# Optimization experiments

Measured on AMD Instinct MI355X. Metric: run time of the kernel, lower is better.

The kernel has to match this reference:

```python
import jax, jax.numpy as jnp
import numpy as np

B, N, E, H = 8, 512, 256, 8
DK = E // H
DIST_BAR = (0.3, 0.7, 1e10)  # init dist_bar + [1e10] appended in forward
NEG = -1e10


def setup_inputs() -> dict:
    key = jax.random.key(0)
    ks = jax.random.split(key, 24)
    s = 0.02
    inp = {
        'query': jax.random.normal(ks[0], (B, N, E), jnp.float32),
        'key':   jax.random.normal(ks[1], (B, N, E), jnp.float32),
        'value': jax.random.normal(ks[2], (B, N, E), jnp.float32),
        'dist':  jax.random.uniform(ks[3], (B, N, N), jnp.float32),
        'mask':  jax.random.randint(ks[4], (B, N, N), 0, 2).astype(jnp.int32),
        # 4 linears (q, k, v, out), stored as [in, out] for x @ W
        'Wq': jax.random.normal(ks[5], (E, E)) * s, 'bq': jnp.zeros((E,)),
        'Wk': jax.random.normal(ks[6], (E, E)) * s, 'bk': jnp.zeros((E,)),
        'Wv': jax.random.normal(ks[7], (E, E)) * s, 'bv': jnp.zeros((E,)),
        'Wo': jax.random.normal(ks[8], (E, E)) * s, 'bo': jnp.zeros((E,)),
        # cnn: Conv2d(1,H,1) -> ReLU -> Conv2d(H,H,1); 1x1 convs = per-pixel linear maps
        'cw1': jax.random.normal(ks[9], (H,)) * s,     'cb1': jnp.zeros((H,)),
        'cw2': jax.random.normal(ks[10], (H, H)) * s,  'cb2': jnp.zeros((H,)),
        # scale_linear: Linear(3E, E) -> ReLU -> Linear(E, E)
        'Ws1': jax.random.normal(ks[11], (3 * E, E)) * s, 'bs1': jnp.zeros((E,)),
        'Ws2': jax.random.normal(ks[12], (E, E)) * s,     'bs2': jnp.zeros((E,)),
    }
    return inp


def reference(query, key, value, dist, mask,
              Wq, bq, Wk, bk, Wv, bv, Wo, bo,
              cw1, cb1, cw2, cb2, Ws1, bs1, Ws2, bs2):
    def heads(x, W, b):  # [B,N,E] -> [B,H,N,DK]
        return (x @ W + b).reshape(B, N, H, DK).transpose(0, 2, 1, 3)

    q, k, v = heads(query, Wq, bq), heads(key, Wk, bk), heads(value, Wv, bv)
    d4 = dist[:, None]  # [B,1,N,N]
    # 1x1 conv stack: [B,1,N,N] -> [B,H,N,N]
    c1 = jax.nn.relu(d4 * cw1[None, :, None, None] + cb1[None, :, None, None])
    dist_conv = jnp.einsum('oi,bijk->bojk', cw2, c1) + cb2[None, :, None, None]

    scores = jnp.einsum('bhqd,bhkd->bhqk', q, k) / np.sqrt(DK).astype(np.float32)
    scores = scores * dist_conv
    scores = jnp.where(mask[:, None] == 0, NEG, scores)

    outs = []
    for bar in DIST_BAR:
        dm = d4 < bar                       # [B,1,N,N] bool
        dm = dm.at[:, :, 0, :].set(True).at[:, :, :, 0].set(True)
        s = jnp.where(dm, scores, NEG)
        p = jax.nn.softmax(s, axis=-1)      # [B,H,N,N]
        o = jnp.einsum('bhqk,bhkd->bhqd', p, v)
        o = o.transpose(0, 2, 1, 3).reshape(B, N, E)
        outs.append(o @ Wo + bo)
    x = jnp.concatenate(outs, axis=-1)      # [B,N,3E]
    h1 = jax.nn.relu(x @ Ws1 + bs1)
    return h1 @ Ws2 + bs2                   # [B,N,E]
```

## Files before the change

kernel.cpp:

```cpp
#include <hip/hip_runtime.h>
#include <math.h>

typedef _Float16 h16;
typedef __attribute__((ext_vector_type(8))) _Float16 h16x8;
typedef __attribute__((ext_vector_type(4))) float f32x4;
typedef unsigned long long u64t;
typedef unsigned int u32t;
typedef unsigned short u16t;
typedef unsigned char u8t;

__global__ void bcomb_k(const float* __restrict__ bo, const float* __restrict__ Ws1,
                        const float* __restrict__ bs1, float* __restrict__ bcomb)
{
    const int jj = threadIdx.x;
    const int r0 = blockIdx.x * 64;
    float acc = (blockIdx.x == 0) ? bs1[jj] : 0.f;
    for (int r = r0; r < r0 + 64; ++r)
        acc = fmaf(bo[r & 255], Ws1[(size_t)r * 256 + jj], acc);
    atomicAdd(&bcomb[jj], acc);
}

__global__ __launch_bounds__(256) void transpose_k(
    const float* __restrict__ Wq, const float* __restrict__ Wk,
    const float* __restrict__ Wv, const float* __restrict__ Ws2,
    const float* __restrict__ Ws1, h16* __restrict__ WT)
{
    const int z = blockIdx.z;
    const float* in = (z == 0) ? Wq : (z == 1) ? Wk : (z == 2) ? Wv :
                      (z == 3) ? Ws2 : (Ws1 + (size_t)(z - 4) * 65536);
    h16* out = WT + (size_t)z * 65536;
    __shared__ float T[32][33];
    const int t = threadIdx.x, tx = t & 31, ty = t >> 5;
    const int r0 = blockIdx.x * 32, c0 = blockIdx.y * 32;
    #pragma unroll
    for (int i = 0; i < 4; ++i) {
        const int row = ty + i * 8;
        T[row][tx] = in[(size_t)(r0 + row) * 256 + c0 + tx];
    }
    __syncthreads();
    #pragma unroll
    for (int i = 0; i < 4; ++i) {
        const int row = ty + i * 8;
        out[(size_t)(c0 + row) * 256 + r0 + tx] = (h16)T[tx][row];
    }
}

template<int A_F32, int MODE>
__global__ __launch_bounds__(256) void hgemm_k(
    const void* __restrict__ Av, const h16* __restrict__ Bt0,
    const float* __restrict__ bias, void* __restrict__ outv,
    int M, int Nn, int K, long btz, int ldt)
{
    const h16* Bt = Bt0 + (size_t)blockIdx.z * btz;
    __shared__ __align__(16) h16 As[64][40];
    __shared__ __align__(16) h16 Bs[64][40];
    const int t = threadIdx.x, w = t >> 6, lane = t & 63;
    const int Q = lane >> 4, n = lane & 15;
    const int row0 = blockIdx.x * 64, col0 = blockIdx.y * 64;
    const int sr = t >> 2, sc = (t & 3) * 8;
    f32x4 acc[4];
    #pragma unroll
    for (int c = 0; c < 4; ++c) acc[c] = (f32x4){0.f, 0.f, 0.f, 0.f};

    for (int k0 = 0; k0 < K; k0 += 32) {
        __syncthreads();
        if (A_F32) {
            const float* ap = (const float*)Av + (size_t)(row0 + sr) * K + k0 + sc;
            float4 f0 = *(const float4*)ap;
            float4 f1 = *(const float4*)(ap + 4);
            h16x8 hv;
            hv[0] = (h16)f0.x; hv[1] = (h16)f0.y; hv[2] = (h16)f0.z; hv[3] = (h16)f0.w;
            hv[4] = (h16)f1.x; hv[5] = (h16)f1.y; hv[6] = (h16)f1.z; hv[7] = (h16)f1.w;
            *(h16x8*)&As[sr][sc] = hv;
        } else {
            *(h16x8*)&As[sr][sc] =
                *(const h16x8*)((const h16*)Av + (size_t)(row0 + sr) * K + k0 + sc);
        }
        *(h16x8*)&Bs[sr][sc] = *(const h16x8*)(Bt + (size_t)(col0 + sr) * K + k0 + sc);
        __syncthreads();
        h16x8 af = *(const h16x8*)&As[w * 16 + n][Q * 8];
        #pragma unroll
        for (int c = 0; c < 4; ++c) {
            h16x8 bf = *(const h16x8*)&Bs[c * 16 + n][Q * 8];
            acc[c] = __builtin_amdgcn_mfma_f32_16x16x32_f16(af, bf, acc[c], 0, 0, 0);
        }
    }

    float bvv[4] = {0.f, 0.f, 0.f, 0.f};
    if (MODE != 4) {
        #pragma unroll
        for (int c = 0; c < 4; ++c) bvv[c] = bias[col0 + c * 16 + n];
    }
    #pragma unroll
    for (int c = 0; c < 4; ++c) {
        #pragma unroll
        for (int r = 0; r < 4; ++r) {
            const int row = row0 + w * 16 + 4 * Q + r;
            const int col = col0 + c * 16 + n;
            if (MODE == 0) {
                ((float*)outv)[(size_t)row * Nn + col] = acc[c][r] + bvv[c];
            } else if (MODE == 2) {
                ((h16*)outv)[(size_t)row * Nn + col] = (h16)fmaxf(acc[c][r] + bvv[c], 0.f);
            } else {
                ((h16*)outv)[(size_t)col * ldt + (int)blockIdx.z * M + row] = (h16)acc[c][r];
            }
        }
    }
}

__global__ __launch_bounds__(256) void qkv_hgemm_k(
    const float* __restrict__ Xq, const float* __restrict__ Xk,
    const float* __restrict__ Xv, const h16* __restrict__ WT,
    const float* __restrict__ bq, const float* __restrict__ bk,
    const float* __restrict__ bv,
    h16* __restrict__ qb, h16* __restrict__ kb, h16* __restrict__ vbT)
{
    const int z = blockIdx.z;
    const float* A    = (z == 0) ? Xq : (z == 1) ? Xk : Xv;
    const h16*   Bt   = WT + (size_t)z * 65536;
    const float* bias = (z == 0) ? bq : (z == 1) ? bk : bv;

    __shared__ __align__(16) h16 As[64][40];
    __shared__ __align__(16) h16 Bs[64][40];
    const int t = threadIdx.x, w = t >> 6, lane = t & 63;
    const int Q = lane >> 4, n = lane & 15;
    const int row0 = blockIdx.x * 64, col0 = blockIdx.y * 64;
    const int sr = t >> 2, sc = (t & 3) * 8;
    f32x4 acc[4];
    #pragma unroll
    for (int c = 0; c < 4; ++c) acc[c] = (f32x4){0.f, 0.f, 0.f, 0.f};

    for (int k0 = 0; k0 < 256; k0 += 32) {
        __syncthreads();
        {
            const float* ap = A + (size_t)(row0 + sr) * 256 + k0 + sc;
            float4 f0 = *(const float4*)ap;
            float4 f1 = *(const float4*)(ap + 4);
            h16x8 hv;
            hv[0] = (h16)f0.x; hv[1] = (h16)f0.y; hv[2] = (h16)f0.z; hv[3] = (h16)f0.w;
            hv[4] = (h16)f1.x; hv[5] = (h16)f1.y; hv[6] = (h16)f1.z; hv[7] = (h16)f1.w;
            *(h16x8*)&As[sr][sc] = hv;
            *(h16x8*)&Bs[sr][sc] = *(const h16x8*)(Bt + (size_t)(col0 + sr) * 256 + k0 + sc);
        }
        __syncthreads();
        h16x8 af = *(const h16x8*)&As[w * 16 + n][Q * 8];
        #pragma unroll
        for (int c = 0; c < 4; ++c) {
            h16x8 bf = *(const h16x8*)&Bs[c * 16 + n][Q * 8];
            acc[c] = __builtin_amdgcn_mfma_f32_16x16x32_f16(af, bf, acc[c], 0, 0, 0);
        }
    }

    float bvv[4];
    #pragma unroll
    for (int c = 0; c < 4; ++c) bvv[c] = bias[col0 + c * 16 + n];

    if (z < 2) {
        h16* out = z ? kb : qb;
        #pragma unroll
        for (int c = 0; c < 4; ++c)
            #pragma unroll
            for (int r = 0; r < 4; ++r)
                out[(size_t)(row0 + w * 16 + 4 * Q + r) * 256 + col0 + c * 16 + n] =
                    (h16)(acc[c][r] + bvv[c]);
    } else {
        const int bb = row0 >> 9;
        #pragma unroll
        for (int c = 0; c < 4; ++c)
            #pragma unroll
            for (int r = 0; r < 4; ++r) {
                const int m = row0 + w * 16 + 4 * Q + r;
                const int col = col0 + c * 16 + n;
                vbT[((size_t)(bb * 256 + col)) * 512 + (m & 511)] = (h16)(acc[c][r] + bvv[c]);
            }
    }
}

__global__ __launch_bounds__(256, 4) void attn_k(
    const h16* __restrict__ qb, const h16* __restrict__ kb,
    const h16* __restrict__ vbT,
    const float* __restrict__ dist, const int* __restrict__ mask,
    const float* __restrict__ cw1, const float* __restrict__ cb1,
    const float* __restrict__ cw2, const float* __restrict__ cb2,
    h16* __restrict__ OB)
{
    const int bx = blockIdx.x, b = bx >> 5, q0 = (bx & 31) * 16;
    const int t = threadIdx.x, w = t >> 6, lane = t & 63;
    const int Q = lane >> 4, n = lane & 15;
    const int h = blockIdx.y * 4 + w;

    __shared__ __align__(16) h16 c1t[16][65][8];
    __shared__ __align__(16) u8t Cd[16][72];
    __shared__ __align__(16) h16 Sx[4][16][72];

    const float invs = 0.17677669529663687f;
    float w1[8], b1[8], w2w[8];
    #pragma unroll
    for (int u = 0; u < 8; ++u) {
        w1[u] = cw1[u]; b1[u] = cb1[u];
        w2w[u] = invs * cw2[h * 8 + u];
    }
    const float fb = invs * cb2[h];

    const h16x8 aq =
        *(const h16x8*)(qb + ((size_t)(b * 512 + q0 + n)) * 256 + h * 32 + Q * 8);

    const f32x4 z4 = {0.f, 0.f, 0.f, 0.f};
    f32x4 acc[3][2];
    #pragma unroll
    for (int s = 0; s < 3; ++s) { acc[s][0] = z4; acc[s][1] = z4; }
    float mprev = -3e38f;
    float lsum[3] = {0.f, 0.f, 0.f};

    const int scol = t & 63, srow0 = t >> 6;

    for (int kc = 0; kc < 8; ++kc) {
        const int kk0 = kc * 64;
        __syncthreads();
        #pragma unroll
        for (int i = 0; i < 4; ++i) {
            const int row = srow0 + 4 * i;
            const size_t off = ((size_t)(b * 512 + q0 + row)) * 512 + kk0 + scol;
            const float d = dist[off];
            const int mk = mask[off];
            const bool fr = ((q0 + row) == 0) || ((kk0 + scol) == 0);
            const bool keep = (mk != 0);
            const u32t code = (keep && (fr || d < 0.3f) ? 1u : 0u)
                            | (keep && (fr || d < 0.7f) ? 2u : 0u)
                            | (keep ? 4u : 0u);
            Cd[row][scol] = (u8t)code;
            h16x8 ch;
            #pragma unroll
            for (int u = 0; u < 8; ++u)
                ch[u] = (h16)fmaxf(fmaf(d, w1[u], b1[u]), 0.f);
            *(h16x8*)&c1t[row][scol][0] = ch;
        }
        __syncthreads();

        f32x4 s4[4];
        #pragma unroll
        for (int cg = 0; cg < 4; ++cg) {
            h16x8 kf = *(const h16x8*)(
                kb + ((size_t)(b * 512 + kk0 + cg * 16 + n)) * 256 + h * 32 + Q * 8);
            s4[cg] = __builtin_amdgcn_mfma_f32_16x16x32_f16(aq, kf, z4, 0, 0, 0);
        }
        #pragma unroll
        for (int cg = 0; cg < 4; ++cg) {
            #pragma unroll
            for (int r = 0; r < 4; ++r) {
                h16x8 ch = *(const h16x8*)&c1t[4 * Q + r][cg * 16 + n][0];
                float f = fb;
                #pragma unroll
                for (int u = 0; u < 8; ++u)
                    f = fmaf((float)ch[u], w2w[u], f);
                Sx[w][4 * Q + r][cg * 16 + n] = (h16)(s4[cg][r] * f);
            }
        }
        __builtin_amdgcn_wave_barrier();

        float sv[16];
        u64t cd0 = *(const u64t*)&Cd[n][Q * 8];
        u64t cd1 = *(const u64t*)&Cd[n][32 + Q * 8];
        {
            h16x8 sh0 = *(const h16x8*)&Sx[w][n][Q * 8];
            h16x8 sh1 = *(const h16x8*)&Sx[w][n][32 + Q * 8];
            #pragma unroll
            for (int j = 0; j < 8; ++j) { sv[j] = (float)sh0[j]; sv[8 + j] = (float)sh1[j]; }
        }
        float cm = -3e38f;
        #pragma unroll
        for (int i = 0; i < 16; ++i) {
            const u32t cc = (u32t)((i < 8 ? cd0 : cd1) >> (8 * (i & 7))) & 7u;
            cm = fmaxf(cm, (cc & 4u) ? sv[i] : -3e38f);
        }
        cm = fmaxf(cm, __shfl_xor(cm, 16));
        cm = fmaxf(cm, __shfl_xor(cm, 32));
        const float mnew = fmaxf(mprev, cm);
        const float alphaA = __expf(mprev - mnew);
        mprev = mnew;

        #pragma unroll
        for (int r = 0; r < 4; ++r) {
            const float aR = __shfl(alphaA, 4 * Q + r);
            #pragma unroll
            for (int s = 0; s < 3; ++s) { acc[s][0][r] *= aR; acc[s][1][r] *= aR; }
        }

        h16x8 pf[3][2];
        float l0 = 0.f, l1 = 0.f, l2 = 0.f;
        #pragma unroll
        for (int i = 0; i < 16; ++i) {
            const u32t cc = (u32t)((i < 8 ? cd0 : cd1) >> (8 * (i & 7))) & 7u;
            const float e = __expf(sv[i] - mnew);
            const float p0 = (cc & 1u) ? e : 0.f;
            const float p1 = (cc & 2u) ? e : 0.f;
            const float p2 = (cc & 4u) ? e : 0.f;
            l0 += p0; l1 += p1; l2 += p2;
            pf[0][i >> 3][i & 7] = (h16)p0;
            pf[1][i >> 3][i & 7] = (h16)p1;
            pf[2][i >> 3][i & 7] = (h16)p2;
        }
        lsum[0] = lsum[0] * alphaA + l0;
        lsum[1] = lsum[1] * alphaA + l1;
        lsum[2] = lsum[2] * alphaA + l2;

        #pragma unroll
        for (int kb2 = 0; kb2 < 2; ++kb2) {
            #pragma unroll
            for (int nh = 0; nh < 2; ++nh) {
                h16x8 vf = *(const h16x8*)(
                    vbT + ((size_t)((b * 8 + h) * 32 + nh * 16 + n)) * 512
                        + kk0 + kb2 * 32 + Q * 8);
                #pragma unroll
                for (int s = 0; s < 3; ++s)
                    acc[s][nh] = __builtin_amdgcn_mfma_f32_16x16x32_f16(
                        pf[s][kb2], vf, acc[s][nh], 0, 0, 0);
            }
        }
    }

    float lrow[3];
    #pragma unroll
    for (int s = 0; s < 3; ++s) {
        float lv = lsum[s];
        lv += __shfl_xor(lv, 16);
        lv += __shfl_xor(lv, 32);
        lrow[s] = lv;
    }
    #pragma unroll
    for (int s = 0; s < 3; ++s) {
        #pragma unroll
        for (int r = 0; r < 4; ++r) {
            const float il = 1.0f / __shfl(lrow[s], 4 * Q + r);
            const size_t row = (size_t)(b * 512 + q0 + 4 * Q + r);
            h16* op = OB + row * 768 + s * 256 + h * 32 + n;
            op[0]  = (h16)(acc[s][0][r] * il);
            op[16] = (h16)(acc[s][1][r] * il);
        }
    }
}

extern "C" void kernel_launch(void* const* d_in, const int* in_sizes, int n_in,
                              void* d_out, int out_size, void* d_ws, size_t ws_size,
                              hipStream_t stream)
{
    const float* query = (const float*)d_in[0];
    const float* key   = (const float*)d_in[1];
    const float* value = (const float*)d_in[2];
    const float* dist  = (const float*)d_in[3];
    const int*   mask  = (const int*)d_in[4];
    const float* Wq = (const float*)d_in[5];  const float* bq = (const float*)d_in[6];
    const float* Wk = (const float*)d_in[7];  const float* bk = (const float*)d_in[8];
    const float* Wv = (const float*)d_in[9];  const float* bv = (const float*)d_in[10];
    const float* Wo = (const float*)d_in[11]; const float* bo = (const float*)d_in[12];
    const float* cw1 = (const float*)d_in[13]; const float* cb1 = (const float*)d_in[14];
    const float* cw2 = (const float*)d_in[15]; const float* cb2 = (const float*)d_in[16];
    const float* Ws1 = (const float*)d_in[17]; const float* bs1 = (const float*)d_in[18];
    const float* Ws2 = (const float*)d_in[19]; const float* bs2 = (const float*)d_in[20];

    h16* qb    = (h16*)d_ws;
    h16* kb    = qb + 1048576;
    h16* vbT   = kb + 1048576;
    h16* OB    = vbT + 1048576;
    h16* h1    = OB + 3145728;
    h16* WT    = h1 + 1048576;
    h16* WbigT = WT + 458752;
    float* bcomb = (float*)(WbigT + 196608);

    hipMemsetAsync(bcomb, 0, 256 * sizeof(float), stream);
    bcomb_k<<<dim3(12), dim3(256), 0, stream>>>(bo, Ws1, bs1, bcomb);

    transpose_k<<<dim3(8, 8, 7), 256, 0, stream>>>(Wq, Wk, Wv, Ws2, Ws1, WT);

    hgemm_k<1, 4><<<dim3(4, 4, 3), 256, 0, stream>>>(
        Wo, WT + 4 * 65536, nullptr, WbigT, 256, 256, 256, 65536, 768);

    qkv_hgemm_k<<<dim3(64, 4, 3), 256, 0, stream>>>(
        query, key, value, WT, bq, bk, bv, qb, kb, vbT);

    attn_k<<<dim3(256, 2), 256, 0, stream>>>(
        qb, kb, vbT, dist, mask, cw1, cb1, cw2, cb2, OB);

    hgemm_k<0, 2><<<dim3(64, 4, 1), 256, 0, stream>>>(
        OB, WbigT, bcomb, h1, 4096, 256, 768, 0, 0);
    hgemm_k<0, 0><<<dim3(64, 4, 1), 256, 0, stream>>>(
        h1, WT + 3 * 65536, bs2, d_out, 4096, 256, 256, 0, 0);
}
```

Before: 193.2 us.

## Merge weight prep and QKV projection into one launch, register-pipeline attention

Drops the separate transpose, bias-combine, memset and weight-fold kernels. Their work now runs inside one merged single-wave-per-block launch that reads the fp32 weights directly with strided per-element loads. The attention kernel no longer stages dist/mask codes and conv features in shared memory with block barriers. It computes the conv factor per element in registers and prefetches the next chunk's K, V, dist and mask into registers, with a double-buffered per-wave score scratch. The final two GEMMs become LDS-free 64-thread kernels. This cuts launch count and block-level synchronisation, but uncoalesced strided weight loads, more conv arithmetic per element, and lower occupancy (launch bounds 256,2) could offset the gains.

```diff
diff --git a/kernel.cpp b/kernel.cpp
--- a/kernel.cpp
+++ b/kernel.cpp
@@ -3,180 +3,116 @@
 
 typedef _Float16 h16;
 typedef __attribute__((ext_vector_type(8))) _Float16 h16x8;
+typedef __attribute__((ext_vector_type(4))) _Float16 h16x4;
 typedef __attribute__((ext_vector_type(4))) float f32x4;
-typedef unsigned long long u64t;
 typedef unsigned int u32t;
-typedef unsigned short u16t;
-typedef unsigned char u8t;
-
-__global__ void bcomb_k(const float* __restrict__ bo, const float* __restrict__ Ws1,
-                        const float* __restrict__ bs1, float* __restrict__ bcomb)
-{
-    const int jj = threadIdx.x;
-    const int r0 = blockIdx.x * 64;
-    float acc = (blockIdx.x == 0) ? bs1[jj] : 0.f;
-    for (int r = r0; r < r0 + 64; ++r)
-        acc = fmaf(bo[r & 255], Ws1[(size_t)r * 256 + jj], acc);
-    atomicAdd(&bcomb[jj], acc);
-}
-
-__global__ __launch_bounds__(256) void transpose_k(
-    const float* __restrict__ Wq, const float* __restrict__ Wk,
-    const float* __restrict__ Wv, const float* __restrict__ Ws2,
-    const float* __restrict__ Ws1, h16* __restrict__ WT)
-{
-    const int z = blockIdx.z;
-    const float* in = (z == 0) ? Wq : (z == 1) ? Wk : (z == 2) ? Wv :
-                      (z == 3) ? Ws2 : (Ws1 + (size_t)(z - 4) * 65536);
-    h16* out = WT + (size_t)z * 65536;
-    __shared__ float T[32][33];
-    const int t = threadIdx.x, tx = t & 31, ty = t >> 5;
-    const int r0 = blockIdx.x * 32, c0 = blockIdx.y * 32;
-    #pragma unroll
-    for (int i = 0; i < 4; ++i) {
-        const int row = ty + i * 8;
-        T[row][tx] = in[(size_t)(r0 + row) * 256 + c0 + tx];
-    }
-    __syncthreads();
-    #pragma unroll
-    for (int i = 0; i < 4; ++i) {
-        const int row = ty + i * 8;
-        out[(size_t)(c0 + row) * 256 + r0 + tx] = (h16)T[tx][row];
-    }
-}
-
-template<int A_F32, int MODE>
-__global__ __launch_bounds__(256) void hgemm_k(
-    const void* __restrict__ Av, const h16* __restrict__ Bt0,
-    const float* __restrict__ bias, void* __restrict__ outv,
-    int M, int Nn, int K, long btz, int ldt)
-{
-    const h16* Bt = Bt0 + (size_t)blockIdx.z * btz;
-    __shared__ __align__(16) h16 As[64][40];
-    __shared__ __align__(16) h16 Bs[64][40];
-    const int t = threadIdx.x, w = t >> 6, lane = t & 63;
+
+__global__ __launch_bounds__(64) void k1_k(
+    const float* __restrict__ query, const float* __restrict__ key,
+    const float* __restrict__ value,
+    const float* __restrict__ Wq, const float* __restrict__ bq,
+    const float* __restrict__ Wk, const float* __restrict__ bk,
+    const float* __restrict__ Wv, const float* __restrict__ bv,
+    const float* __restrict__ Wo, const float* __restrict__ bo,
+    const float* __restrict__ Ws1, const float* __restrict__ bs1,
+    h16* __restrict__ qb, h16* __restrict__ kb, h16* __restrict__ vbT,
+    h16* __restrict__ WbigT, float* __restrict__ bcomb)
+{
+    const int bid = blockIdx.x, lane = threadIdx.x;
     const int Q = lane >> 4, n = lane & 15;
-    const int row0 = blockIdx.x * 64, col0 = blockIdx.y * 64;
-    const int sr = t >> 2, sc = (t & 3) * 8;
-    f32x4 acc[4];
-    #pragma unroll
-    for (int c = 0; c < 4; ++c) acc[c] = (f32x4){0.f, 0.f, 0.f, 0.f};
-
-    for (int k0 = 0; k0 < K; k0 += 32) {
-        __syncthreads();
-        if (A_F32) {
-            const float* ap = (const float*)Av + (size_t)(row0 + sr) * K + k0 + sc;
-            float4 f0 = *(const float4*)ap;
-            float4 f1 = *(const float4*)(ap + 4);
-            h16x8 hv;
-            hv[0] = (h16)f0.x; hv[1] = (h16)f0.y; hv[2] = (h16)f0.z; hv[3] = (h16)f0.w;
-            hv[4] = (h16)f1.x; hv[5] = (h16)f1.y; hv[6] = (h16)f1.z; hv[7] = (h16)f1.w;
-            *(h16x8*)&As[sr][sc] = hv;
+    const f32x4 z4 = {0.f, 0.f, 0.f, 0.f};
+
+    if (bid < 3072) {
+        const int z = bid >> 10, tt = bid & 1023;
+        const int row0 = (tt & 255) << 4, col0 = (tt >> 8) << 6;
+        const float* A    = (z == 0) ? query : (z == 1) ? key : value;
+        const float* W    = (z == 0) ? Wq : (z == 1) ? Wk : Wv;
+        const float* bias = (z == 0) ? bq : (z == 1) ? bk : bv;
+
+        f32x4 acc[4] = {z4, z4, z4, z4};
+        #pragma unroll 2
+        for (int k0 = 0; k0 < 256; k0 += 32) {
+            const float* ap = A + (size_t)(row0 + n) * 256 + k0 + Q * 8;
+            float4 a0 = *(const float4*)ap, a1 = *(const float4*)(ap + 4);
+            h16x8 af;
+            af[0] = (h16)a0.x; af[1] = (h16)a0.y; af[2] = (h16)a0.z; af[3] = (h16)a0.w;
+            af[4] = (h16)a1.x; af[5] = (h16)a1.y; af[6] = (h16)a1.z; af[7] = (h16)a1.w;
+            #pragma unroll
+            for (int cg = 0; cg < 4; ++cg) {
+                const int col = col0 + cg * 16 + n;
+                h16x8 bf;
+                #pragma unroll
+                for (int j = 0; j < 8; ++j)
+                    bf[j] = (h16)W[(size_t)(k0 + Q * 8 + j) * 256 + col];
+                acc[cg] = __builtin_amdgcn_mfma_f32_16x16x32_f16(af, bf, acc[cg], 0, 0, 0);
+            }
+        }
+        if (z < 2) {
+            h16* out = z ? kb : qb;
+            #pragma unroll
+            for (int cg = 0; cg < 4; ++cg) {
+                const int col = col0 + cg * 16 + n;
+                const float bvv = bias[col];
+                #pragma unroll
+                for (int r = 0; r < 4; ++r)
+                    out[(size_t)(row0 + 4 * Q + r) * 256 + col] = (h16)(acc[cg][r] + bvv);
+            }
         } else {
-            *(h16x8*)&As[sr][sc] =
-                *(const h16x8*)((const h16*)Av + (size_t)(row0 + sr) * K + k0 + sc);
-        }
-        *(h16x8*)&Bs[sr][sc] = *(const h16x8*)(Bt + (size_t)(col0 + sr) * K + k0 + sc);
-        __syncthreads();
-        h16x8 af = *(const h16x8*)&As[w * 16 + n][Q * 8];
-        #pragma unroll
-        for (int c = 0; c < 4; ++c) {
-            h16x8 bf = *(const h16x8*)&Bs[c * 16 + n][Q * 8];
-            acc[c] = __builtin_amdgcn_mfma_f32_16x16x32_f16(af, bf, acc[c], 0, 0, 0);
-        }
-    }
-
-    float bvv[4] = {0.f, 0.f, 0.f, 0.f};
-    if (MODE != 4) {
-        #pragma unroll
-        for (int c = 0; c < 4; ++c) bvv[c] = bias[col0 + c * 16 + n];
-    }
-    #pragma unroll
-    for (int c = 0; c < 4; ++c) {
-        #pragma unroll
-        for (int r = 0; r < 4; ++r) {
-            const int row = row0 + w * 16 + 4 * Q + r;
-            const int col = col0 + c * 16 + n;
-            if (MODE == 0) {
-                ((float*)outv)[(size_t)row * Nn + col] = acc[c][r] + bvv[c];
-            } else if (MODE == 2) {
-                ((h16*)outv)[(size_t)row * Nn + col] = (h16)fmaxf(acc[c][r] + bvv[c], 0.f);
-            } else {
-                ((h16*)outv)[(size_t)col * ldt + (int)blockIdx.z * M + row] = (h16)acc[c][r];
-            }
-        }
-    }
-}
-
-__global__ __launch_bounds__(256) void qkv_hgemm_k(
-    const float* __restrict__ Xq, const float* __restrict__ Xk,
-    const float* __restrict__ Xv, const h16* __restrict__ WT,
-    const float* __restrict__ bq, const float* __restrict__ bk,
-    const float* __restrict__ bv,
-    h16* __restrict__ qb, h16* __restrict__ kb, h16* __restrict__ vbT)
-{
-    const int z = blockIdx.z;
-    const float* A    = (z == 0) ? Xq : (z == 1) ? Xk : Xv;
-    const h16*   Bt   = WT + (size_t)z * 65536;
-    const float* bias = (z == 0) ? bq : (z == 1) ? bk : bv;
-
-    __shared__ __align__(16) h16 As[64][40];
-    __shared__ __align__(16) h16 Bs[64][40];
-    const int t = threadIdx.x, w = t >> 6, lane = t & 63;
-    const int Q = lane >> 4, n = lane & 15;
-    const int row0 = blockIdx.x * 64, col0 = blockIdx.y * 64;
-    const int sr = t >> 2, sc = (t & 3) * 8;
-    f32x4 acc[4];
-    #pragma unroll
-    for (int c = 0; c < 4; ++c) acc[c] = (f32x4){0.f, 0.f, 0.f, 0.f};
-
-    for (int k0 = 0; k0 < 256; k0 += 32) {
-        __syncthreads();
-        {
-            const float* ap = A + (size_t)(row0 + sr) * 256 + k0 + sc;
-            float4 f0 = *(const float4*)ap;
-            float4 f1 = *(const float4*)(ap + 4);
-            h16x8 hv;
-            hv[0] = (h16)f0.x; hv[1] = (h16)f0.y; hv[2] = (h16)f0.z; hv[3] = (h16)f0.w;
-            hv[4] = (h16)f1.x; hv[5] = (h16)f1.y; hv[6] = (h16)f1.z; hv[7] = (h16)f1.w;
-            *(h16x8*)&As[sr][sc] = hv;
-            *(h16x8*)&Bs[sr][sc] = *(const h16x8*)(Bt + (size_t)(col0 + sr) * 256 + k0 + sc);
-        }
-        __syncthreads();
-        h16x8 af = *(const h16x8*)&As[w * 16 + n][Q * 8];
-        #pragma unroll
-        for (int c = 0; c < 4; ++c) {
-            h16x8 bf = *(const h16x8*)&Bs[c * 16 + n][Q * 8];
-            acc[c] = __builtin_amdgcn_mfma_f32_16x16x32_f16(af, bf, acc[c], 0, 0, 0);
-        }
-    }
-
-    float bvv[4];
-    #pragma unroll
-    for (int c = 0; c < 4; ++c) bvv[c] = bias[col0 + c * 16 + n];
-
-    if (z < 2) {
-        h16* out = z ? kb : qb;
-        #pragma unroll
-        for (int c = 0; c < 4; ++c)
-            #pragma unroll
-            for (int r = 0; r < 4; ++r)
-                out[(size_t)(row0 + w * 16 + 4 * Q + r) * 256 + col0 + c * 16 + n] =
-                    (h16)(acc[c][r] + bvv[c]);
+            const int bb = row0 >> 9, tok0 = (row0 & 511) + 4 * Q;
+            #pragma unroll
+            for (int cg = 0; cg < 4; ++cg) {
+                const int col = col0 + cg * 16 + n;
+                const int hh = col >> 5, dd = col & 31;
+                const float bvv = bias[col];
+                h16x4 pk;
+                #pragma unroll
+                for (int r = 0; r < 4; ++r) pk[r] = (h16)(acc[cg][r] + bvv);
+                *(h16x4*)(vbT + ((size_t)((bb * 8 + hh) * 32 + dd)) * 512 + tok0) = pk;
+            }
+        }
+    } else if (bid < 3264) {
+        const int idx = bid - 3072;
+        const int sgm = idx >> 6, tt = idx & 63;
+        const int row0 = (tt & 15) << 4, col0 = (tt >> 4) << 6;
+        const float* Bsrc = Ws1 + (size_t)sgm * 65536;
+
+        f32x4 acc[4] = {z4, z4, z4, z4};
+        #pragma unroll 2
+        for (int k0 = 0; k0 < 256; k0 += 32) {
+            const float* ap = Wo + (size_t)(row0 + n) * 256 + k0 + Q * 8;
+            float4 a0 = *(const float4*)ap, a1 = *(const float4*)(ap + 4);
+            h16x8 af;
+            af[0] = (h16)a0.x; af[1] = (h16)a0.y; af[2] = (h16)a0.z; af[3] = (h16)a0.w;
+            af[4] = (h16)a1.x; af[5] = (h16)a1.y; af[6] = (h16)a1.z; af[7] = (h16)a1.w;
+            #pragma unroll
+            for (int cg = 0; cg < 4; ++cg) {
+                const int col = col0 + cg * 16 + n;
+                h16x8 bf;
+                #pragma unroll
+                for (int j = 0; j < 8; ++j)
+                    bf[j] = (h16)Bsrc[(size_t)(k0 + Q * 8 + j) * 256 + col];
+                acc[cg] = __builtin_amdgcn_mfma_f32_16x16x32_f16(af, bf, acc[cg], 0, 0, 0);
+            }
+        }
+        #pragma unroll
+        for (int cg = 0; cg < 4; ++cg) {
+            const int col = col0 + cg * 16 + n;
+            h16x4 pk;
+            #pragma unroll
+            for (int r = 0; r < 4; ++r) pk[r] = (h16)acc[cg][r];
+            *(h16x4*)(WbigT + (size_t)col * 768 + sgm * 256 + row0 + 4 * Q) = pk;
+        }
     } else {
-        const int bb = row0 >> 9;
-        #pragma unroll
-        for (int c = 0; c < 4; ++c)
-            #pragma unroll
-            for (int r = 0; r < 4; ++r) {
-                const int m = row0 + w * 16 + 4 * Q + r;
-                const int col = col0 + c * 16 + n;
-                vbT[((size_t)(bb * 256 + col)) * 512 + (m & 511)] = (h16)(acc[c][r] + bvv[c]);
-            }
-    }
-}
-
-__global__ __launch_bounds__(256, 4) void attn_k(
+        const int col = ((bid - 3264) << 6) + lane;
+        float acc = bs1[col];
+        #pragma unroll 16
+        for (int r = 0; r < 768; ++r)
+            acc = fmaf(bo[r & 255], Ws1[(size_t)r * 256 + col], acc);
+        bcomb[col] = acc;
+    }
+}
+
+__global__ __launch_bounds__(256, 2) void attn_k(
     const h16* __restrict__ qb, const h16* __restrict__ kb,
     const h16* __restrict__ vbT,
     const float* __restrict__ dist, const int* __restrict__ mask,
@@ -185,13 +121,12 @@
     h16* __restrict__ OB)
 {
     const int bx = blockIdx.x, b = bx >> 5, q0 = (bx & 31) * 16;
+    const int hg = blockIdx.y;
     const int t = threadIdx.x, w = t >> 6, lane = t & 63;
     const int Q = lane >> 4, n = lane & 15;
-    const int h = blockIdx.y * 4 + w;
-
-    __shared__ __align__(16) h16 c1t[16][65][8];
-    __shared__ __align__(16) u8t Cd[16][72];
-    __shared__ __align__(16) h16 Sx[4][16][72];
+    const int h = hg * 4 + w;
+
+    __shared__ __align__(16) h16 Sx[4][2][16][76];
 
     const float invs = 0.17677669529663687f;
     float w1[8], b1[8], w2w[8];
@@ -209,69 +144,90 @@
     f32x4 acc[3][2];
     #pragma unroll
     for (int s = 0; s < 3; ++s) { acc[s][0] = z4; acc[s][1] = z4; }
-    float mprev = -3e38f;
-    float lsum[3] = {0.f, 0.f, 0.f};
-
-    const int scol = t & 63, srow0 = t >> 6;
-
+    float mprev = -3e38f, lsum[3] = {0.f, 0.f, 0.f};
+
+    const size_t dmrow = ((size_t)(b * 512 + q0 + n)) * 512 + Q * 8;
+    const size_t kbase = ((size_t)(b * 512)) * 256 + h * 32 + Q * 8;
+    const size_t vbase = ((size_t)((b * 8 + h) * 32 + n)) * 512 + Q * 8;
+    const bool qz = (q0 + n) == 0;
+
+    h16x8 kf[4], vf[4];
+    float4 df[4]; int4 mf[4];
+    #pragma unroll
+    for (int cg = 0; cg < 4; ++cg)
+        kf[cg] = *(const h16x8*)(kb + kbase + (size_t)(cg * 16 + n) * 256);
+    #pragma unroll
+    for (int nh = 0; nh < 2; ++nh)
+        #pragma unroll
+        for (int k2 = 0; k2 < 2; ++k2)
+            vf[nh * 2 + k2] = *(const h16x8*)(vbT + vbase + nh * 16 * 512 + k2 * 32);
+    df[0] = *(const float4*)(dist + dmrow);
+    df[1] = *(const float4*)(dist + dmrow + 4);
+    df[2] = *(const float4*)(dist + dmrow + 32);
+    df[3] = *(const float4*)(dist + dmrow + 36);
+    mf[0] = *(const int4*)(mask + dmrow);
+    mf[1] = *(const int4*)(mask + dmrow + 4);
+    mf[2] = *(const int4*)(mask + dmrow + 32);
+    mf[3] = *(const int4*)(mask + dmrow + 36);
+
+    #pragma unroll 1
     for (int kc = 0; kc < 8; ++kc) {
-        const int kk0 = kc * 64;
-        __syncthreads();
-        #pragma unroll
-        for (int i = 0; i < 4; ++i) {
-            const int row = srow0 + 4 * i;
-            const size_t off = ((size_t)(b * 512 + q0 + row)) * 512 + kk0 + scol;
-            const float d = dist[off];
-            const int mk = mask[off];
-            const bool fr = ((q0 + row) == 0) || ((kk0 + scol) == 0);
-            const bool keep = (mk != 0);
-            const u32t code = (keep && (fr || d < 0.3f) ? 1u : 0u)
-                            | (keep && (fr || d < 0.7f) ? 2u : 0u)
-                            | (keep ? 4u : 0u);
-            Cd[row][scol] = (u8t)code;
-            h16x8 ch;
+        const int kk0 = kc * 64, cb_ = kc & 1;
+
+        h16x8 kfN[4], vfN[4]; float4 dfN[4]; int4 mfN[4];
+        if (kc < 7) {
+            const int kn = kk0 + 64;
+            #pragma unroll
+            for (int cg = 0; cg < 4; ++cg)
+                kfN[cg] = *(const h16x8*)(kb + kbase + (size_t)(kn + cg * 16 + n) * 256);
+            #pragma unroll
+            for (int nh = 0; nh < 2; ++nh)
+                #pragma unroll
+                for (int k2 = 0; k2 < 2; ++k2)
+                    vfN[nh * 2 + k2] =
+                        *(const h16x8*)(vbT + vbase + nh * 16 * 512 + kn + k2 * 32);
+            dfN[0] = *(const float4*)(dist + dmrow + kn);
+            dfN[1] = *(const float4*)(dist + dmrow + kn + 4);
+            dfN[2] = *(const float4*)(dist + dmrow + kn + 32);
+            dfN[3] = *(const float4*)(dist + dmrow + kn + 36);
+            mfN[0] = *(const int4*)(mask + dmrow + kn);
+            mfN[1] = *(const int4*)(mask + dmrow + kn + 4);
+            mfN[2] = *(const int4*)(mask + dmrow + kn + 32);
+            mfN[3] = *(const int4*)(mask + dmrow + kn + 36);
+        }
+
+        f32x4 s4[4];
+        #pragma unroll
+        for (int cg = 0; cg < 4; ++cg)
+            s4[cg] = __builtin_amdgcn_mfma_f32_16x16x32_f16(aq, kf[cg], z4, 0, 0, 0);
+        #pragma unroll
+        for (int cg = 0; cg < 4; ++cg)
+            #pragma unroll
+            for (int r = 0; r < 4; ++r)
+                Sx[w][cb_][4 * Q + r][cg * 16 + n] = (h16)s4[cg][r];
+        __builtin_amdgcn_wave_barrier();
+        const h16x8 sh0 = *(const h16x8*)&Sx[w][cb_][n][Q * 8];
+        const h16x8 sh1 = *(const h16x8*)&Sx[w][cb_][n][32 + Q * 8];
+        __builtin_amdgcn_wave_barrier();
+
+        float sv[16]; bool in0[16], in1[16];
+        float cm = -3e38f;
+        #pragma unroll
+        for (int i = 0; i < 16; ++i) {
+            const float d = ((i & 8) ? df[2 + ((i >> 2) & 1)] : df[(i >> 2) & 1])[i & 3];
+            const int  mk = ((i & 8) ? mf[2 + ((i >> 2) & 1)] : mf[(i >> 2) & 1])[i & 3];
+            float f = fb;
             #pragma unroll
             for (int u = 0; u < 8; ++u)
-                ch[u] = (h16)fmaxf(fmaf(d, w1[u], b1[u]), 0.f);
-            *(h16x8*)&c1t[row][scol][0] = ch;
-        }
-        __syncthreads();
-
-        f32x4 s4[4];
-        #pragma unroll
-        for (int cg = 0; cg < 4; ++cg) {
-            h16x8 kf = *(const h16x8*)(
-                kb + ((size_t)(b * 512 + kk0 + cg * 16 + n)) * 256 + h * 32 + Q * 8);
-            s4[cg] = __builtin_amdgcn_mfma_f32_16x16x32_f16(aq, kf, z4, 0, 0, 0);
-        }
-        #pragma unroll
-        for (int cg = 0; cg < 4; ++cg) {
-            #pragma unroll
-            for (int r = 0; r < 4; ++r) {
-                h16x8 ch = *(const h16x8*)&c1t[4 * Q + r][cg * 16 + n][0];
-                float f = fb;
-                #pragma unroll
-                for (int u = 0; u < 8; ++u)
-                    f = fmaf((float)ch[u], w2w[u], f);
-                Sx[w][4 * Q + r][cg * 16 + n] = (h16)(s4[cg][r] * f);
-            }
-        }
-        __builtin_amdgcn_wave_barrier();
-
-        float sv[16];
-        u64t cd0 = *(const u64t*)&Cd[n][Q * 8];
-        u64t cd1 = *(const u64t*)&Cd[n][32 + Q * 8];
-        {
-            h16x8 sh0 = *(const h16x8*)&Sx[w][n][Q * 8];
-            h16x8 sh1 = *(const h16x8*)&Sx[w][n][32 + Q * 8];
-            #pragma unroll
-            for (int j = 0; j < 8; ++j) { sv[j] = (float)sh0[j]; sv[8 + j] = (float)sh1[j]; }
-        }
-        float cm = -3e38f;
-        #pragma unroll
-        for (int i = 0; i < 16; ++i) {
-            const u32t cc = (u32t)((i < 8 ? cd0 : cd1) >> (8 * (i & 7))) & 7u;
-            cm = fmaxf(cm, (cc & 4u) ? sv[i] : -3e38f);
+                f = fmaf(fmaxf(fmaf(d, w1[u], b1[u]), 0.f), w2w[u], f);
+            const float sraw = (float)((i < 8) ? sh0[i] : sh1[i & 7]);
+            const int kg = kk0 + ((i < 8) ? (Q * 8 + i) : (32 + Q * 8 + (i & 7)));
+            const bool fr = qz || (kg == 0);
+            const float s = (mk != 0) ? sraw * f : -3e38f;
+            sv[i] = s;
+            in0[i] = fr || (d < 0.3f);
+            in1[i] = fr || (d < 0.7f);
+            cm = fmaxf(cm, s);
         }
         cm = fmaxf(cm, __shfl_xor(cm, 16));
         cm = fmaxf(cm, __shfl_xor(cm, 32));
@@ -286,35 +242,37 @@
             for (int s = 0; s < 3; ++s) { acc[s][0][r] *= aR; acc[s][1][r] *= aR; }
         }
 
-        h16x8 pf[3][2];
         float l0 = 0.f, l1 = 0.f, l2 = 0.f;
         #pragma unroll
-        for (int i = 0; i < 16; ++i) {
-            const u32t cc = (u32t)((i < 8 ? cd0 : cd1) >> (8 * (i & 7))) & 7u;
-            const float e = __expf(sv[i] - mnew);
-            const float p0 = (cc & 1u) ? e : 0.f;
-            const float p1 = (cc & 2u) ? e : 0.f;
-            const float p2 = (cc & 4u) ? e : 0.f;
-            l0 += p0; l1 += p1; l2 += p2;
-            pf[0][i >> 3][i & 7] = (h16)p0;
-            pf[1][i >> 3][i & 7] = (h16)p1;
-            pf[2][i >> 3][i & 7] = (h16)p2;
+        for (int k2 = 0; k2 < 2; ++k2) {
+            h16x8 pf0, pf1, pf2;
+            #pragma unroll
+            for (int j = 0; j < 8; ++j) {
+                const int i = k2 * 8 + j;
+                const float e = __expf(sv[i] - mnew);
+                const float p0 = in0[i] ? e : 0.f;
+                const float p1 = in1[i] ? e : 0.f;
+                l0 += p0; l1 += p1; l2 += e;
+                pf0[j] = (h16)p0; pf1[j] = (h16)p1; pf2[j] = (h16)e;
+            }
+            #pragma unroll
+            for (int nh = 0; nh < 2; ++nh) {
+                acc[0][nh] = __builtin_amdgcn_mfma_f32_16x16x32_f16(
+                    pf0, vf[nh * 2 + k2], acc[0][nh], 0, 0, 0);
+                acc[1][nh] = __builtin_amdgcn_mfma_f32_16x16x32_f16(
+                    pf1, vf[nh * 2 + k2], acc[1][nh], 0, 0, 0);
+                acc[2][nh] = __builtin_amdgcn_mfma_f32_16x16x32_f16(
+                    pf2, vf[nh * 2 + k2], acc[2][nh], 0, 0, 0);
+            }
         }
         lsum[0] = lsum[0] * alphaA + l0;
         lsum[1] = lsum[1] * alphaA + l1;
         lsum[2] = lsum[2] * alphaA + l2;
 
-        #pragma unroll
-        for (int kb2 = 0; kb2 < 2; ++kb2) {
-            #pragma unroll
-            for (int nh = 0; nh < 2; ++nh) {
-                h16x8 vf = *(const h16x8*)(
-                    vbT + ((size_t)((b * 8 + h) * 32 + nh * 16 + n)) * 512
-                        + kk0 + kb2 * 32 + Q * 8);
-                #pragma unroll
-                for (int s = 0; s < 3; ++s)
-                    acc[s][nh] = __builtin_amdgcn_mfma_f32_16x16x32_f16(
-                        pf[s][kb2], vf, acc[s][nh], 0, 0, 0);
+        if (kc < 7) {
+            #pragma unroll
+            for (int i = 0; i < 4; ++i) {
+                kf[i] = kfN[i]; vf[i] = vfN[i]; df[i] = dfN[i]; mf[i] = mfN[i];
             }
         }
     }
@@ -337,6 +295,66 @@
             op[0]  = (h16)(acc[s][0][r] * il);
             op[16] = (h16)(acc[s][1][r] * il);
         }
+    }
+}
+
+__global__ __launch_bounds__(64) void g1_k(
+    const h16* __restrict__ OB, const h16* __restrict__ WbigT,
+    const float* __restrict__ bcomb, h16* __restrict__ h1)
+{
+    const int lane = threadIdx.x, Q = lane >> 4, n = lane & 15;
+    const int row0 = (blockIdx.x & 255) << 4, col0 = (blockIdx.x >> 8) << 6;
+    const f32x4 z4 = {0.f, 0.f, 0.f, 0.f};
+    f32x4 acc[4] = {z4, z4, z4, z4};
+
+    #pragma unroll 4
+    for (int k0 = 0; k0 < 768; k0 += 32) {
+        h16x8 af = *(const h16x8*)(OB + (size_t)(row0 + n) * 768 + k0 + Q * 8);
+        #pragma unroll
+        for (int cg = 0; cg < 4; ++cg) {
+            h16x8 bf = *(const h16x8*)(WbigT + (size_t)(col0 + cg * 16 + n) * 768 + k0 + Q * 8);
+            acc[cg] = __builtin_amdgcn_mfma_f32_16x16x32_f16(af, bf, acc[cg], 0, 0, 0);
+        }
+    }
+    #pragma unroll
+    for (int cg = 0; cg < 4; ++cg) {
+        const int col = col0 + cg * 16 + n;
+        const float bvv = bcomb[col];
+        #pragma unroll
+        for (int r = 0; r < 4; ++r)
+            h1[(size_t)(row0 + 4 * Q + r) * 256 + col] = (h16)fmaxf(acc[cg][r] + bvv, 0.f);
+    }
+}
+
+__global__ __launch_bounds__(64) void g2_k(
+    const h16* __restrict__ h1, const float* __restrict__ Ws2,
+    const float* __restrict__ bs2, float* __restrict__ out)
+{
+    const int lane = threadIdx.x, Q = lane >> 4, n = lane & 15;
+    const int row0 = (blockIdx.x & 255) << 4, col0 = (blockIdx.x >> 8) << 6;
+    const f32x4 z4 = {0.f, 0.f, 0.f, 0.f};
+    f32x4 acc[4] = {z4, z4, z4, z4};
+
+    #pragma unroll 2
+    for (int k0 = 0; k0 < 256; k0 += 32) {
+        h16x8 af = *(const h16x8*)(h1 + (size_t)(row0 + n) * 256 + k0 + Q * 8);
+        #pragma unroll
+        for (int cg = 0; cg < 4; ++cg) {
+            const int col = col0 + cg * 16 + n;
+            h16x8 bf;
+            #pragma unroll
+            for (int j = 0; j < 8; ++j)
+                bf[j] = (h16)Ws2[(size_t)(k0 + Q * 8 + j) * 256 + col];
+            acc[cg] = __builtin_amdgcn_mfma_f32_16x16x32_f16(af, bf, acc[cg], 0, 0, 0);
+        }
+    }
+    #pragma unroll
+    for (int cg = 0; cg < 4; ++cg) {
+        const int col = col0 + cg * 16 + n;
+        const float bvv = bs2[col];
+        #pragma unroll
+        for (int r = 0; r < 4; ++r)
+            out[(size_t)(row0 + 4 * Q + r) * 256 + col] = acc[cg][r] + bvv;
     }
 }
 
@@ -363,26 +381,16 @@
     h16* vbT   = kb + 1048576;
     h16* OB    = vbT + 1048576;
     h16* h1    = OB + 3145728;
-    h16* WT    = h1 + 1048576;
-    h16* WbigT = WT + 458752;
+    h16* WbigT = h1 + 1048576;
     float* bcomb = (float*)(WbigT + 196608);
 
-    hipMemsetAsync(bcomb, 0, 256 * sizeof(float), stream);
-    bcomb_k<<<dim3(12), dim3(256), 0, stream>>>(bo, Ws1, bs1, bcomb);
-
-    transpose_k<<<dim3(8, 8, 7), 256, 0, stream>>>(Wq, Wk, Wv, Ws2, Ws1, WT);
-
-    hgemm_k<1, 4><<<dim3(4, 4, 3), 256, 0, stream>>>(
-        Wo, WT + 4 * 65536, nullptr, WbigT, 256, 256, 256, 65536, 768);
-
-    qkv_hgemm_k<<<dim3(64, 4, 3), 256, 0, stream>>>(
-        query, key, value, WT, bq, bk, bv, qb, kb, vbT);
-
-    attn_k<<<dim3(256, 2), 256, 0, stream>>>(
-        qb, kb, vbT, dist, mask, cw1, cb1, cw2, cb2, OB);
-
-    hgemm_k<0, 2><<<dim3(64, 4, 1), 256, 0, stream>>>(
-        OB, WbigT, bcomb, h1, 4096, 256, 768, 0, 0);
-    hgemm_k<0, 0><<<dim3(64, 4, 1), 256, 0, stream>>>(
-        h1, WT + 3 * 65536, bs2, d_out, 4096, 256, 256, 0, 0);
-}
+    k1_k<<<dim3(3268), 64, 0, stream>>>(query, key, value, Wq, bq, Wk, bk,
+                                        Wv, bv, Wo, bo, Ws1, bs1,
+                                        qb, kb, vbT, WbigT, bcomb);
+
+    attn_k<<<dim3(256, 2), 256, 0, stream>>>(qb, kb, vbT, dist, mask,
+                                             cw1, cb1, cw2, cb2, OB);
+
+    g1_k<<<dim3(1024), 64, 0, stream>>>(OB, WbigT, bcomb, h1);
+    g2_k<<<dim3(1024), 64, 0, stream>>>(h1, Ws2, bs2, (float*)d_out);
+}
```

Result: slower. 244.0 us (+26.3%).
